# Optimization experiments

Measured on AMD Instinct MI355X. Metric: run time of the kernel, lower is better.

Reference implementation:

```python
import jax, jax.numpy as jnp
import numpy as np

N_NODE = 200000
HIDDEN = 128
BATCH = 1024
SEQ = 50
NNZ = 3200000
HG_STEPS = 3
LINE_STEPS = 3
BETA = 0.01
POS_MAX = 200


def setup_inputs() -> dict:
    key = jax.random.key(0)
    ks = jax.random.split(key, 20)
    stdv = 1.0 / np.sqrt(HIDDEN)
    u = lambda k, shp: jax.random.uniform(k, shp, jnp.float32, -stdv, stdv)
    inp = {
        "items_emb": u(ks[0], (N_NODE, HIDDEN)),
        "pos_table": u(ks[1], (POS_MAX, HIDDEN)),
        "w1_W": u(ks[2], (2 * HIDDEN, HIDDEN)), "w1_b": u(ks[3], (HIDDEN,)),
        "w2_W": u(ks[4], (HIDDEN, HIDDEN)), "w2_b": u(ks[5], (HIDDEN,)),
        "w3_W": u(ks[6], (HIDDEN, HIDDEN)), "w3_b": u(ks[7], (HIDDEN,)),
        "f_T": u(ks[8], (HIDDEN, 1)),
        "hg_vals": jax.random.uniform(ks[9], (NNZ,), jnp.float32),
        "line_adj_matrix": jax.random.uniform(ks[10], (BATCH, BATCH), jnp.float32),
        "degree": jax.random.uniform(ks[11], (BATCH, BATCH), jnp.float32),
        "hg_rows": jax.random.randint(ks[12], (NNZ,), 0, N_NODE, jnp.int32),
        "hg_cols": jax.random.randint(ks[13], (NNZ,), 0, N_NODE, jnp.int32),
        "session_info": jax.random.randint(ks[14], (BATCH, SEQ), 0, N_NODE, jnp.int64),
        "reversed_info": jax.random.randint(ks[15], (BATCH, SEQ), 0, N_NODE, jnp.int64),
        "sessions_len": jax.random.randint(ks[16], (BATCH,), 1, SEQ + 1, jnp.int32),
        "masks": jnp.ones((BATCH, SEQ), dtype=bool),
        "perm_row": jax.random.permutation(ks[17], BATCH).astype(jnp.int32),
        "perm_col": jax.random.permutation(ks[18], HIDDEN).astype(jnp.int32),
    }
    return inp


def _hypergraph_conv(rows, cols, vals, x):
    embs = x
    acc = x
    for _ in range(HG_STEPS):
        embs = jax.ops.segment_sum(vals[:, None] * embs[cols], rows, num_segments=N_NODE)
        acc = acc + embs
    return acc / (HG_STEPS + 1)


def _generate_hg_emb(item_emb, sessions_len, reversed_info, masks,
                     pos_table, w1_W, w1_b, w2_W, w2_b, w3_W, w3_b, f_T):
    padded = jnp.concatenate([jnp.zeros((1, HIDDEN), jnp.float32), item_emb], 0)
    seq_h = padded[reversed_info]                       # [B, L, H]
    L = seq_h.shape[1]
    slen = sessions_len.astype(jnp.float32)[:, None]
    sess_mean = jnp.sum(seq_h, 1) / slen                # [B, H]
    pos = pos_table[:L][None, :, :]                     # [1, L, H]
    new_seq = jnp.tanh(jnp.concatenate([jnp.broadcast_to(pos, seq_h.shape), seq_h], -1) @ w1_W + w1_b)
    gate = jax.nn.sigmoid((sess_mean @ w2_W + w2_b)[:, None, :] + new_seq @ w3_W + w3_b)
    alpha = (gate @ f_T) * masks.astype(jnp.float32)[:, :, None]   # [B, L, 1]
    theta = jnp.sum(alpha * new_seq, 1)                 # [B, H]
    return theta


def _line_graph_conv(D, A, items_emb, session_info, sessions_len):
    DA = D @ A
    padded = jnp.concatenate([jnp.zeros((1, HIDDEN), jnp.float32), items_emb], 0)
    sess = jnp.sum(padded[session_info], 1) / sessions_len.astype(jnp.float32)[:, None]
    acc = sess
    cur = sess
    for _ in range(LINE_STEPS):
        cur = DA @ cur
        acc = acc + cur
    return acc / (LINE_STEPS + 1)


def _ssl(hg_sess, line_sess, perm_row, perm_col):
    pos = jnp.sum(hg_sess * line_sess, 1)
    corrupted = hg_sess[perm_row][:, perm_col]
    neg = jnp.sum(corrupted * line_sess, 1)
    eps = 1e-08
    return jnp.sum(-jnp.log(eps + jax.nn.sigmoid(pos)) - jnp.log(eps + (1.0 - jax.nn.sigmoid(neg))))


def reference(items_emb, pos_table, w1_W, w1_b, w2_W, w2_b, w3_W, w3_b, f_T,
              hg_vals, line_adj_matrix, degree,
              hg_rows, hg_cols, session_info, reversed_info, sessions_len,
              masks, perm_row, perm_col):
    hg_item = _hypergraph_conv(hg_rows, hg_cols, hg_vals, items_emb)
    hg_sess = _generate_hg_emb(hg_item, sessions_len, reversed_info, masks,
                               pos_table, w1_W, w1_b, w2_W, w2_b, w3_W, w3_b, f_T)
    line_sess = _line_graph_conv(degree, line_adj_matrix, items_emb, session_info, sessions_len)
    cl_loss = BETA * _ssl(hg_sess, line_sess, perm_row, perm_col)
    return hg_sess, cl_loss, hg_item
```

## Files before the change

kernel.cpp:

```cpp
#include <hip/hip_runtime.h>
#include <hip/hip_fp16.h>
#include <cstdint>
#include <cstddef>

#define NN   200000
#define HH   128
#define BB   1024
#define LL   50
#define NNZK 3200000
#define RPBK 200
#define NBK  1000
#define MSB  256
#define CHUNK (NNZK/MSB)
#define SK   8

typedef unsigned int uint32;
typedef unsigned short ushort16;
typedef __attribute__((ext_vector_type(8))) short bf16x8;
typedef __attribute__((ext_vector_type(4))) float f32x4;
union U8 { uint32 u[4]; bf16x8 v; };

#if defined(__has_builtin)
#if __has_builtin(__builtin_amdgcn_cvt_pk_f32_fp8) && __has_builtin(__builtin_amdgcn_cvt_pk_fp8_f32)
#define HW_FP8 1
#endif
#endif
#ifndef HW_FP8
#define HW_FP8 0
#endif

__device__ __forceinline__ uint32 f2bf2(float a, float b){
  uint32 ua=__float_as_uint(a), ub=__float_as_uint(b);
  ua = (ua + 0x7FFFu + ((ua>>16)&1u)) >> 16;
  ub = (ub + 0x7FFFu + ((ub>>16)&1u)) >> 16;
  return ua | (ub<<16);
}
__device__ __forceinline__ float2 bf2x2f(uint32 u){
  return make_float2(__uint_as_float(u<<16), __uint_as_float(u & 0xFFFF0000u));
}

#if !HW_FP8
__device__ __forceinline__ uint32 enc8_sw(float f){
  ushort16 b = __half_as_ushort(__float2half_rn(f*0.00390625f));
  uint32 t = b & 0x7FFFu;
  uint32 r = (t + 0x3Fu + ((t>>7)&1u)) >> 7;
  if(r > 0x7Eu) r = 0x7Eu;
  return ((b>>8)&0x80u) | r;
}
#endif

__device__ __forceinline__ float2 fp8x2f(uint32 s){
#if HW_FP8
  auto r = __builtin_amdgcn_cvt_pk_f32_fp8((int)s, false);
  return make_float2(r[0], r[1]);
#else
  union{uint32 u; __half2 h;} cv;
  cv.u = ((s&0x80u)<<8)|((s&0x7Fu)<<7) | ((s&0x8000u)<<16)|((s&0x7F00u)<<15);
  float2 f = __half22float2(cv.h);
  return make_float2(f.x*256.f, f.y*256.f);
#endif
}

__device__ __forceinline__ ushort16 f2fp8x2(float a, float b){
#if HW_FP8
  return (ushort16)__builtin_amdgcn_cvt_pk_fp8_f32(a, b, 0, false);
#else
  return (ushort16)(enc8_sw(a) | (enc8_sw(b)<<8));
#endif
}

__device__ __forceinline__ uint32 f2fp8x4(float4 v){
#if HW_FP8
  int p = __builtin_amdgcn_cvt_pk_fp8_f32(v.x, v.y, 0, false);
  p = __builtin_amdgcn_cvt_pk_fp8_f32(v.z, v.w, p, true);
  return (uint32)p;
#else
  return enc8_sw(v.x) | (enc8_sw(v.y)<<8) | (enc8_sw(v.z)<<16) | (enc8_sw(v.w)<<24);
#endif
}

__global__ __launch_bounds__(256) void k_cvt_bhist(const float* __restrict__ x,
    uint32* __restrict__ obf, uint32* __restrict__ o8,
    const int* __restrict__ rows, int* __restrict__ bhist, int* __restrict__ bh2){
  if(blockIdx.x < MSB){
    __shared__ int h[NBK];
    for(int b=threadIdx.x;b<NBK;b+=256) h[b]=0;
    __syncthreads();
    const int i0=blockIdx.x*CHUNK;
    for(int i=i0+threadIdx.x;i<i0+CHUNK;i+=256) atomicAdd(&h[rows[i]/RPBK],1);
    __syncthreads();
    for(int b=threadIdx.x;b<NBK;b+=256){
      int c=h[b];
      bh2[blockIdx.x*NBK+b]=c;
      if(c) atomicAdd(&bhist[b],c);
    }
  } else {
    const int n = NN*32;
    const int nb = gridDim.x - MSB;
    for(int i=(blockIdx.x-MSB)*256+threadIdx.x; i<n; i+=nb*256){
      float4 v = ((const float4*)x)[i];
      obf[2*i]   = f2bf2(v.x, v.y);
      obf[2*i+1] = f2bf2(v.z, v.w);
      o8[i] = f2fp8x4(v);
    }
  }
}

__global__ __launch_bounds__(1024) void k_bscan(const int* __restrict__ bhist,
    int* __restrict__ bstart, int* __restrict__ bcur){
  __shared__ int s[1024];
  int t=threadIdx.x;
  int v=(t<NBK)?bhist[t]:0;
  s[t]=v;
  __syncthreads();
  for(int off=1;off<1024;off<<=1){
    int u=(t>=off)?s[t-off]:0; __syncthreads(); s[t]+=u; __syncthreads();
  }
  if(t<NBK){ int e=s[t]-v; bstart[t]=e; bcur[t]=e; }
}

__global__ __launch_bounds__(256) void k_msplit(const int* __restrict__ rows,
    const int* __restrict__ cols, const float* __restrict__ vals,
    const int* __restrict__ bh2, int* __restrict__ bcur, int2* __restrict__ bpk){
  __shared__ int hist[NBK];
  __shared__ int rbase[NBK];
  const int tid=threadIdx.x;
  const int i0=blockIdx.x*CHUNK, i1=i0+CHUNK;
  for(int b=tid;b<NBK;b+=256){
    int c=bh2[blockIdx.x*NBK+b];
    rbase[b] = c ? atomicAdd(&bcur[b],c) : 0;
    hist[b]=0;
  }
  __syncthreads();
  for(int i=i0+tid;i<i1;i+=256){
    int r=rows[i];
    int b=r/RPBK, ro=r-b*RPBK;
    int p = rbase[b] + atomicAdd(&hist[b],1);
    bpk[p]=make_int2(cols[i] | (ro<<18), __float_as_int(vals[i]));
  }
}

__global__ __launch_bounds__(256) void k_bucket_sort(const int2* __restrict__ bpk,
    const int* __restrict__ bstart, const int* __restrict__ bhist,
    int2* __restrict__ pk, int* __restrict__ rp){
  __shared__ int cnt[RPBK];
  __shared__ int sc[256];
  int b=blockIdx.x, t=threadIdx.x;
  int base=bstart[b], total=bhist[b];
  if(t<RPBK) cnt[t]=0;
  __syncthreads();
  for(int j=t;j<total;j+=256) atomicAdd(&cnt[((uint32)bpk[base+j].x)>>18],1);
  __syncthreads();
  int myc=(t<RPBK)?cnt[t]:0;
  sc[t]=myc;
  __syncthreads();
  for(int off=1;off<256;off<<=1){
    int u=(t>=off)?sc[t-off]:0; __syncthreads(); sc[t]+=u; __syncthreads();
  }
  int excl = sc[t]-myc;
  __syncthreads();
  if(t<RPBK){ cnt[t]=base+excl; rp[b*RPBK+t]=base+excl; }
  if(b==0 && t==0) rp[NN]=NNZK;
  __syncthreads();
  for(int j=t;j<total;j+=256){
    int2 e=bpk[base+j];
    int ro=((uint32)e.x)>>18;
    int p=atomicAdd(&cnt[ro],1);
    pk[p]=make_int2((e.x&0x3FFFF)<<7, e.y);
  }
}

__device__ __forceinline__ void spmm_body(const int2* __restrict__ pk, int j0, int j1,
    const char* __restrict__ src, int lane2, float& ax, float& ay){
  int j  = __builtin_amdgcn_readfirstlane(j0);
  int jE = __builtin_amdgcn_readfirstlane(j1);
  for(; j+16<=jE; j+=16){
    int2 p[16]; ushort16 e[16];
    #pragma unroll
    for(int u=0;u<16;++u) p[u]=pk[j+u];
    #pragma unroll
    for(int u=0;u<16;++u) e[u]=*(const ushort16*)(src + (uint32)__builtin_amdgcn_readfirstlane(p[u].x) + lane2);
    #pragma unroll
    for(int u=0;u<16;++u){
      float2 f=fp8x2f(e[u]);
      float v=__int_as_float(p[u].y);
      ax=fmaf(v,f.x,ax); ay=fmaf(v,f.y,ay);
    }
  }
  for(; j+8<=jE; j+=8){
    int2 p[8]; ushort16 e[8];
    #pragma unroll
    for(int u=0;u<8;++u) p[u]=pk[j+u];
    #pragma unroll
    for(int u=0;u<8;++u) e[u]=*(const ushort16*)(src + (uint32)__builtin_amdgcn_readfirstlane(p[u].x) + lane2);
    #pragma unroll
    for(int u=0;u<8;++u){
      float2 f=fp8x2f(e[u]);
      float v=__int_as_float(p[u].y);
      ax=fmaf(v,f.x,ax); ay=fmaf(v,f.y,ay);
    }
  }
  for(; j+4<=jE; j+=4){
    int2 p[4]; ushort16 e[4];
    #pragma unroll
    for(int u=0;u<4;++u) p[u]=pk[j+u];
    #pragma unroll
    for(int u=0;u<4;++u) e[u]=*(const ushort16*)(src + (uint32)__builtin_amdgcn_readfirstlane(p[u].x) + lane2);
    #pragma unroll
    for(int u=0;u<4;++u){
      float2 f=fp8x2f(e[u]);
      float v=__int_as_float(p[u].y);
      ax=fmaf(v,f.x,ax); ay=fmaf(v,f.y,ay);
    }
  }
  for(; j<jE; ++j){
    int2 p=pk[j];
    float2 f=fp8x2f(*(const ushort16*)(src + (uint32)__builtin_amdgcn_readfirstlane(p.x) + lane2));
    float v=__int_as_float(p.y);
    ax=fmaf(v,f.x,ax); ay=fmaf(v,f.y,ay);
  }
}

__global__ __launch_bounds__(256) void k_spmm_b(
    const int2* __restrict__ pk, const int* __restrict__ rp,
    const ushort16* __restrict__ src, ushort16* __restrict__ dst)
{
  int wid = blockIdx.x*4 + (threadIdx.x>>6);
  int lane = threadIdx.x & 63;
  if(wid>=NN) return;
  float ax=0.f, ay=0.f;
  spmm_body(pk, rp[wid], rp[wid+1], (const char*)src, lane*2, ax, ay);
  dst[(size_t)wid*64+lane]=f2fp8x2(ax,ay);
}

__global__ __launch_bounds__(256) void k_spmm_final(
    const int2* __restrict__ pk, const int* __restrict__ rp,
    const ushort16* __restrict__ A8, const ushort16* __restrict__ B8,
    const uint32* xbf, float* __restrict__ acc, uint32* obf)
{
  int wid = blockIdx.x*4 + (threadIdx.x>>6);
  int lane = threadIdx.x & 63;
  if(wid>=NN) return;
  float ax=0.f, ay=0.f;
  spmm_body(pk, rp[wid], rp[wid+1], (const char*)B8, lane*2, ax, ay);
  float2 xv  = bf2x2f(xbf[(size_t)wid*64+lane]);
  float2 e1v = fp8x2f(A8[(size_t)wid*64+lane]);
  float2 e2v = fp8x2f(B8[(size_t)wid*64+lane]);
  size_t ao=(size_t)wid*128 + lane*2;
  float rx = (xv.x + e1v.x + e2v.x + ax)*0.25f;
  float ry = (xv.y + e1v.y + e2v.y + ay)*0.25f;
  acc[ao]=rx; acc[ao+1]=ry;
  obf[(size_t)wid*64+lane]=f2bf2(rx,ry);
}

__global__ __launch_bounds__(128) void k_sessmean2(const uint32* __restrict__ hgbf,
    const int* __restrict__ rev, const int* __restrict__ slen,
    const float* __restrict__ w2, const float* __restrict__ b2, float* __restrict__ sm2,
    const float* __restrict__ pos_table, const float* __restrict__ w1W,
    const float* __restrict__ w1b0, float* __restrict__ posW1,
    const float* __restrict__ items, const int* __restrict__ sinfo,
    float* __restrict__ cur, float* __restrict__ accL){
  __shared__ float sm[HH];
  int b=blockIdx.x, h=threadIdx.x;
  int hw=h>>1, hi=h&1;
  float sl=1.f/(float)slen[b];
  {
    float s=0.f;
    for(int l=0;l<LL;++l){
      int idx=sinfo[b*LL+l];
      if(idx>0 && idx<=NN) s += items[(size_t)(idx-1)*HH+h];
    }
    s *= sl;
    cur[(size_t)b*HH+h]=s; accL[(size_t)b*HH+h]=s;
  }
  float s=0.f;
  for(int l=0;l<LL;++l){
    int idx=rev[b*LL+l];
    if(idx>0 && idx<=NN){
      float2 f=bf2x2f(hgbf[(size_t)(idx-1)*64+hw]);
      s += hi ? f.y : f.x;
    }
  }
  sm[h]=s*sl;
  __syncthreads();
  float a=b2[h];
  for(int k=0;k<HH;++k) a=fmaf(sm[k], w2[k*HH+h], a);
  sm2[b*HH+h]=a;
  if(b<LL){
    float pa=w1b0[h];
    for(int k=0;k<HH;++k) pa=fmaf(pos_table[b*HH+k], w1W[k*HH+h], pa);
    posW1[b*HH+h]=pa;
  }
}

#define AS 69
#define BS 67
__global__ __launch_bounds__(256) void k_nsgemm(
    const uint32* __restrict__ hgbf, const int* __restrict__ rev,
    const float* __restrict__ w1b, const float* __restrict__ posW1,
    float* __restrict__ ns)
{
  __shared__ uint32 sA[64*AS];
  __shared__ uint32 sB[128*BS];
  const int tid=threadIdx.x;
  {
    int r=tid>>2, p=tid&3;
    int idx = rev[blockIdx.x*64 + r];
    if(idx>0 && idx<=NN){
      const uint32* s = hgbf + (size_t)(idx-1)*64 + p*16;
      #pragma unroll
      for(int j=0;j<16;++j) sA[r*AS+p*16+j]=s[j];
    } else {
      #pragma unroll
      for(int j=0;j<16;++j) sA[r*AS+p*16+j]=0u;
    }
  }
  for(int i=tid;i<128*64;i+=256){
    int n=i&127, kp=i>>7;
    sB[n*BS+kp]=f2bf2(w1b[(2*kp)*HH+n], w1b[(2*kp+1)*HH+n]);
  }
  __syncthreads();
  const int w=tid>>6, lane=tid&63, g=lane>>4, m15=lane&15;
  f32x4 acc[8];
  #pragma unroll
  for(int nt=0;nt<8;++nt) acc[nt]=(f32x4){0.f,0.f,0.f,0.f};
  #pragma unroll
  for(int kt=0;kt<4;++kt){
    U8 a;
    int ab=(w*16+m15)*AS + kt*16 + g*4;
    a.u[0]=sA[ab]; a.u[1]=sA[ab+1]; a.u[2]=sA[ab+2]; a.u[3]=sA[ab+3];
    #pragma unroll
    for(int nt=0;nt<8;++nt){
      U8 b;
      int bb=(nt*16+m15)*BS + kt*16 + g*4;
      b.u[0]=sB[bb]; b.u[1]=sB[bb+1]; b.u[2]=sB[bb+2]; b.u[3]=sB[bb+3];
      acc[nt]=__builtin_amdgcn_mfma_f32_16x16x32_bf16(a.v,b.v,acc[nt],0,0,0);
    }
  }
  int rowbase = blockIdx.x*64 + w*16 + g*4;
  #pragma unroll
  for(int r=0;r<4;++r){
    int gr=rowbase+r;
    int l=gr%LL;
    #pragma unroll
    for(int nt=0;nt<8;++nt){
      int col=nt*16+m15;
      ns[(size_t)gr*HH+col] = tanhf(acc[nt][r] + posW1[l*HH+col]);
    }
  }
}

__global__ __launch_bounds__(256) void k_agemm(
    const float* __restrict__ ns, const float* __restrict__ w3,
    const float* __restrict__ sm2, const float* __restrict__ b3,
    const float* __restrict__ fT, float* __restrict__ alpha)
{
  __shared__ uint32 sA[64*AS];
  __shared__ uint32 sB[128*BS];
  const int tid=threadIdx.x;
  {
    int r=tid>>2, p=tid&3;
    const float2* s = (const float2*)(ns + (size_t)(blockIdx.x*64+r)*HH + p*32);
    #pragma unroll
    for(int j=0;j<16;++j){ float2 f=s[j]; sA[r*AS+p*16+j]=f2bf2(f.x,f.y); }
  }
  for(int i=tid;i<128*64;i+=256){
    int n=i&127, kp=i>>7;
    sB[n*BS+kp]=f2bf2(w3[(2*kp)*HH+n], w3[(2*kp+1)*HH+n]);
  }
  __syncthreads();
  const int w=tid>>6, lane=tid&63, g=lane>>4, m15=lane&15;
  f32x4 acc[8];
  #pragma unroll
  for(int nt=0;nt<8;++nt) acc[nt]=(f32x4){0.f,0.f,0.f,0.f};
  #pragma unroll
  for(int kt=0;kt<4;++kt){
    U8 a;
    int ab=(w*16+m15)*AS + kt*16 + g*4;
    a.u[0]=sA[ab]; a.u[1]=sA[ab+1]; a.u[2]=sA[ab+2]; a.u[3]=sA[ab+3];
    #pragma unroll
    for(int nt=0;nt<8;++nt){
      U8 b;
      int bb=(nt*16+m15)*BS + kt*16 + g*4;
      b.u[0]=sB[bb]; b.u[1]=sB[bb+1]; b.u[2]=sB[bb+2]; b.u[3]=sB[bb+3];
      acc[nt]=__builtin_amdgcn_mfma_f32_16x16x32_bf16(a.v,b.v,acc[nt],0,0,0);
    }
  }
  int rowbase = blockIdx.x*64 + w*16 + g*4;
  #pragma unroll
  for(int r=0;r<4;++r){
    int gr=rowbase+r;
    int b_=gr/LL;
    float rsum=0.f;
    #pragma unroll
    for(int nt=0;nt<8;++nt){
      int col=nt*16+m15;
      float gv = acc[nt][r] + sm2[b_*HH+col] + b3[col];
      rsum += fT[col] / (1.f + expf(-gv));
    }
    rsum += __shfl_xor(rsum,1);
    rsum += __shfl_xor(rsum,2);
    rsum += __shfl_xor(rsum,4);
    rsum += __shfl_xor(rsum,8);
    if(m15==0) alpha[gr]=rsum;
  }
}

__global__ __launch_bounds__(128) void k_theta(const float* __restrict__ ns,
    const float* __restrict__ alpha, float* __restrict__ hg_sess){
  __shared__ float sal[64];
  int b=blockIdx.x, h=threadIdx.x;
  if(h<LL) sal[h]=alpha[b*LL+h];
  __syncthreads();
  float t=0.f;
  for(int l=0;l<LL;++l) t=fmaf(sal[l], ns[((size_t)b*LL+l)*HH+h], t);
  hg_sess[(size_t)b*HH+h]=t;
}

__global__ __launch_bounds__(128) void k_matpart(const float* __restrict__ M,
    const float* __restrict__ src, float* __restrict__ part){
  int rq = blockIdx.x >> 3;
  int kc = blockIdx.x & 7;
  int h = threadIdx.x;
  int r0 = rq*4;
  const int KC = BB/SK;
  const float* m0 = M + (size_t)r0*BB + kc*KC;
  const float* m1 = m0 + BB;
  const float* m2 = m1 + BB;
  const float* m3 = m2 + BB;
  const float* s0 = src + (size_t)kc*KC*HH + h;
  float a0=0,a1=0,a2=0,a3=0;
  for(int k=0;k<KC;++k){
    float s=s0[(size_t)k*HH];
    a0=fmaf(m0[k],s,a0); a1=fmaf(m1[k],s,a1);
    a2=fmaf(m2[k],s,a2); a3=fmaf(m3[k],s,a3);
  }
  size_t o=(size_t)kc*BB*HH + (size_t)r0*HH + h;
  part[o]=a0; part[o+HH]=a1; part[o+2*HH]=a2; part[o+3*HH]=a3;
}

__global__ __launch_bounds__(256) void k_matcomb(const float* __restrict__ part,
    float* __restrict__ dst, float* __restrict__ acc, int mode){
  int i = blockIdx.x*256+threadIdx.x;
  const int S = BB*HH;
  float v = 0.f;
  #pragma unroll
  for(int kc=0;kc<SK;++kc) v += part[i+(size_t)kc*S];
  dst[i]=v;
  if(mode==1) acc[i]+=v;
  else if(mode==2) acc[i]=(acc[i]+v)*0.25f;
}

__global__ __launch_bounds__(128) void k_ssl(const float* __restrict__ hg,
    const float* __restrict__ line, const int* __restrict__ pr,
    const int* __restrict__ pc, float* __restrict__ part){
  int b=blockIdx.x, h=threadIdx.x;
  __shared__ float sp[2][2];
  float lv = line[(size_t)b*HH+h];
  float v1 = hg[(size_t)b*HH+h]*lv;
  float v2 = hg[(size_t)pr[b]*HH + pc[h]]*lv;
  for(int o=32;o>0;o>>=1){ v1+=__shfl_xor(v1,o); v2+=__shfl_xor(v2,o); }
  int wv=h>>6, ln=h&63;
  if(ln==0){ sp[0][wv]=v1; sp[1][wv]=v2; }
  __syncthreads();
  if(h==0){
    float pos=sp[0][0]+sp[0][1];
    float neg=sp[1][0]+sp[1][1];
    float sigp=1.f/(1.f+expf(-pos));
    float sign_=1.f/(1.f+expf(-neg));
    part[b] = -logf(1e-8f+sigp) - logf(1e-8f+(1.f-sign_));
  }
}

__global__ __launch_bounds__(256) void k_red(const float* __restrict__ part, float* __restrict__ loss){
  __shared__ float s[256];
  int t=threadIdx.x;
  s[t]=part[t]+part[t+256]+part[t+512]+part[t+768];
  __syncthreads();
  for(int o=128;o>0;o>>=1){ if(t<o) s[t]+=s[t+o]; __syncthreads(); }
  if(t==0) *loss = 0.01f*s[0];
}

extern "C" void kernel_launch(void* const* d_in, const int* in_sizes, int n_in,
                              void* d_out, int out_size, void* d_ws, size_t ws_size,
                              hipStream_t stream){
  const float* items    =(const float*)d_in[0];
  const float* pos_table=(const float*)d_in[1];
  const float* w1W      =(const float*)d_in[2];
  const float* w1b_     =(const float*)d_in[3];
  const float* w2W      =(const float*)d_in[4];
  const float* w2b      =(const float*)d_in[5];
  const float* w3W      =(const float*)d_in[6];
  const float* w3b      =(const float*)d_in[7];
  const float* fT       =(const float*)d_in[8];
  const float* hvals    =(const float*)d_in[9];
  const float* lineA    =(const float*)d_in[10];
  const float* degD     =(const float*)d_in[11];
  const int*   hrows    =(const int*)d_in[12];
  const int*   hcols    =(const int*)d_in[13];
  const int*   sinfo    =(const int*)d_in[14];
  const int*   rinfo    =(const int*)d_in[15];
  const int*   slen     =(const int*)d_in[16];
  const int*   prow     =(const int*)d_in[18];
  const int*   pcol     =(const int*)d_in[19];

  float* outf   = (float*)d_out;
  float* hg_sess= outf;
  float* loss   = outf + (size_t)BB*HH;
  float* hgout  = outf + (size_t)BB*HH + 1;

  char* base=(char*)d_ws; size_t off=0;
  auto carve=[&](size_t bytes)->char*{ char* p=base+off; off=(off+bytes+255)&~(size_t)255; return p; };

  float*    posW1 =(float*)   carve((size_t)LL*HH*4);
  float*    curA  =(float*)   carve((size_t)BB*HH*4);
  float*    curB  =(float*)   carve((size_t)BB*HH*4);
  float*    tmpv  =(float*)   carve((size_t)BB*HH*4);
  float*    accL  =(float*)   carve((size_t)BB*HH*4);
  float*    lpart =(float*)   carve((size_t)BB*4);
  float*    mpart =(float*)   carve((size_t)SK*BB*HH*4);
  int2*     pk    =(int2*)    carve((size_t)NNZK*8);
  int*      rp    =(int*)     carve((size_t)(NN+1)*4);
  int*      bhist =(int*)     carve((size_t)NBK*4);
  int*      bstart=(int*)     carve((size_t)NBK*4);
  int*      bcur  =(int*)     carve((size_t)NBK*4);
  int*      bh2   =(int*)     carve((size_t)MSB*NBK*4);
  uint32*   itbf  =(uint32*)  carve((size_t)NN*64*4);
  uint32*   it8   =(uint32*)  carve((size_t)NN*32*4);
  ushort16* A8    =(ushort16*)carve((size_t)NN*64*2);
  ushort16* B8    =(ushort16*)carve((size_t)NN*64*2);
  if(off > ws_size) return;

  int2*   bpk   = (int2*)A8;
  uint32* hgbf  = itbf;
  float*  ns    = (float*)A8;
  float*  alpha = ns + (size_t)BB*LL*HH;
  float*  sm2   = alpha + (size_t)BB*LL;

  hipMemsetAsync(bhist,0,(size_t)NBK*4,stream);
  k_cvt_bhist<<<MSB+2048,256,0,stream>>>(items,itbf,it8,hrows,bhist,bh2);
  k_bscan<<<1,1024,0,stream>>>(bhist,bstart,bcur);
  k_msplit<<<MSB,256,0,stream>>>(hrows,hcols,hvals,bh2,bcur,bpk);
  k_bucket_sort<<<NBK,256,0,stream>>>(bpk,bstart,bhist,pk,rp);

  k_spmm_b    <<<NN/4,256,0,stream>>>(pk,rp, (const ushort16*)it8, A8);
  k_spmm_b    <<<NN/4,256,0,stream>>>(pk,rp, A8, B8);
  k_spmm_final<<<NN/4,256,0,stream>>>(pk,rp, A8, B8, itbf, hgout, hgbf);

  k_sessmean2<<<BB,HH,0,stream>>>(hgbf,rinfo,slen,w2W,w2b,sm2,
                                  pos_table,w1W,w1b_,posW1,
                                  items,sinfo,curA,accL);
  k_nsgemm   <<<(BB*LL)/64,256,0,stream>>>(hgbf,rinfo,w1W+HH*HH,posW1,ns);
  k_agemm    <<<(BB*LL)/64,256,0,stream>>>(ns,w3W,sm2,w3b,fT,alpha);
  k_theta    <<<BB,HH,0,stream>>>(ns,alpha,hg_sess);

  for(int s=0;s<3;++s){
    float* srcv=(s&1)?curB:curA;
    float* dstv=(s&1)?curA:curB;
    k_matpart<<<(BB/4)*SK,128,0,stream>>>(lineA,srcv,mpart);
    k_matcomb<<<BB*HH/256,256,0,stream>>>(mpart,tmpv,nullptr,0);
    k_matpart<<<(BB/4)*SK,128,0,stream>>>(degD,tmpv,mpart);
    k_matcomb<<<BB*HH/256,256,0,stream>>>(mpart,dstv,accL,(s==2)?2:1);
  }

  k_ssl<<<BB,HH,0,stream>>>(hg_sess,accL,prow,pcol,lpart);
  k_red<<<1,256,0,stream>>>(lpart,loss);
}
```

Before: 602.1 us.

## Split SpMM wavefront into four nonzero groups with 8-byte fp8 loads

The SpMM kernels now split each row's wavefront into four 16-lane groups. Each group handles a different nonzero, loads 8 fp8 values (8 bytes) per lane, and accumulates 8 partial sums. The groups are then combined with cross-lane shuffles and only group 0 writes the output. The aim is to keep four independent gathers in flight per wavefront instead of one serialized wide gather per nonzero, improving memory-level parallelism on the random gathers. The cost is extra shuffle reductions, more registers, and three-quarters of the lanes idle during the epilogue.

```diff
diff --git a/kernel.cpp b/kernel.cpp
--- a/kernel.cpp
+++ b/kernel.cpp
@@ -170,87 +170,100 @@
   }
 }
 
-__device__ __forceinline__ void spmm_body(const int2* __restrict__ pk, int j0, int j1,
-    const char* __restrict__ src, int lane2, float& ax, float& ay){
+__device__ __forceinline__ void q_acc(float* ax, uint2 e, float v){
+  float2 f0=fp8x2f(e.x), f1=fp8x2f(e.x>>16);
+  float2 f2=fp8x2f(e.y), f3=fp8x2f(e.y>>16);
+  ax[0]=fmaf(v,f0.x,ax[0]); ax[1]=fmaf(v,f0.y,ax[1]);
+  ax[2]=fmaf(v,f1.x,ax[2]); ax[3]=fmaf(v,f1.y,ax[3]);
+  ax[4]=fmaf(v,f2.x,ax[4]); ax[5]=fmaf(v,f2.y,ax[5]);
+  ax[6]=fmaf(v,f3.x,ax[6]); ax[7]=fmaf(v,f3.y,ax[7]);
+}
+
+__device__ __forceinline__ void spmm_body_q(const int2* __restrict__ pk, int j0, int j1,
+    const char* __restrict__ src, int goff, int grp, float* ax){
   int j  = __builtin_amdgcn_readfirstlane(j0);
   int jE = __builtin_amdgcn_readfirstlane(j1);
   for(; j+16<=jE; j+=16){
-    int2 p[16]; ushort16 e[16];
-    #pragma unroll
-    for(int u=0;u<16;++u) p[u]=pk[j+u];
-    #pragma unroll
-    for(int u=0;u<16;++u) e[u]=*(const ushort16*)(src + (uint32)__builtin_amdgcn_readfirstlane(p[u].x) + lane2);
-    #pragma unroll
-    for(int u=0;u<16;++u){
-      float2 f=fp8x2f(e[u]);
-      float v=__int_as_float(p[u].y);
-      ax=fmaf(v,f.x,ax); ay=fmaf(v,f.y,ay);
-    }
-  }
-  for(; j+8<=jE; j+=8){
-    int2 p[8]; ushort16 e[8];
-    #pragma unroll
-    for(int u=0;u<8;++u) p[u]=pk[j+u];
-    #pragma unroll
-    for(int u=0;u<8;++u) e[u]=*(const ushort16*)(src + (uint32)__builtin_amdgcn_readfirstlane(p[u].x) + lane2);
-    #pragma unroll
-    for(int u=0;u<8;++u){
-      float2 f=fp8x2f(e[u]);
-      float v=__int_as_float(p[u].y);
-      ax=fmaf(v,f.x,ax); ay=fmaf(v,f.y,ay);
-    }
+    int2 p[4]; uint2 e[4];
+    #pragma unroll
+    for(int u=0;u<4;++u) p[u]=pk[j+4*u+grp];
+    #pragma unroll
+    for(int u=0;u<4;++u) e[u]=*(const uint2*)(src + (uint32)p[u].x + goff);
+    #pragma unroll
+    for(int u=0;u<4;++u) q_acc(ax, e[u], __int_as_float(p[u].y));
   }
   for(; j+4<=jE; j+=4){
-    int2 p[4]; ushort16 e[4];
-    #pragma unroll
-    for(int u=0;u<4;++u) p[u]=pk[j+u];
-    #pragma unroll
-    for(int u=0;u<4;++u) e[u]=*(const ushort16*)(src + (uint32)__builtin_amdgcn_readfirstlane(p[u].x) + lane2);
-    #pragma unroll
-    for(int u=0;u<4;++u){
-      float2 f=fp8x2f(e[u]);
-      float v=__int_as_float(p[u].y);
-      ax=fmaf(v,f.x,ax); ay=fmaf(v,f.y,ay);
-    }
-  }
-  for(; j<jE; ++j){
-    int2 p=pk[j];
-    float2 f=fp8x2f(*(const ushort16*)(src + (uint32)__builtin_amdgcn_readfirstlane(p.x) + lane2));
-    float v=__int_as_float(p.y);
-    ax=fmaf(v,f.x,ax); ay=fmaf(v,f.y,ay);
+    int2 p=pk[j+grp];
+    uint2 e=*(const uint2*)(src + (uint32)p.x + goff);
+    q_acc(ax, e, __int_as_float(p.y));
+  }
+  int rem = jE - j;
+  if(rem>0){
+    int jj = j + (grp<rem ? grp : 0);
+    int2 p=pk[jj];
+    float v = (grp<rem) ? __int_as_float(p.y) : 0.f;
+    uint2 e=*(const uint2*)(src + (uint32)p.x + goff);
+    q_acc(ax, e, v);
+  }
+}
+
+__device__ __forceinline__ void q_reduce(float* ax){
+  #pragma unroll
+  for(int k=0;k<8;++k){
+    ax[k] += __shfl_xor(ax[k],16);
+    ax[k] += __shfl_xor(ax[k],32);
   }
 }
 
 __global__ __launch_bounds__(256) void k_spmm_b(
     const int2* __restrict__ pk, const int* __restrict__ rp,
-    const ushort16* __restrict__ src, ushort16* __restrict__ dst)
+    const char* __restrict__ src, uint32* __restrict__ dst)
 {
   int wid = blockIdx.x*4 + (threadIdx.x>>6);
   int lane = threadIdx.x & 63;
   if(wid>=NN) return;
-  float ax=0.f, ay=0.f;
-  spmm_body(pk, rp[wid], rp[wid+1], (const char*)src, lane*2, ax, ay);
-  dst[(size_t)wid*64+lane]=f2fp8x2(ax,ay);
+  int grp=lane>>4, goff=(lane&15)*8;
+  float ax[8]={0,0,0,0,0,0,0,0};
+  spmm_body_q(pk, rp[wid], rp[wid+1], src, goff, grp, ax);
+  q_reduce(ax);
+  if(grp==0){
+    uint2 o;
+    o.x=f2fp8x4(make_float4(ax[0],ax[1],ax[2],ax[3]));
+    o.y=f2fp8x4(make_float4(ax[4],ax[5],ax[6],ax[7]));
+    *(uint2*)((char*)dst + (size_t)wid*128 + goff) = o;
+  }
 }
 
 __global__ __launch_bounds__(256) void k_spmm_final(
     const int2* __restrict__ pk, const int* __restrict__ rp,
-    const ushort16* __restrict__ A8, const ushort16* __restrict__ B8,
+    const char* __restrict__ A8, const char* __restrict__ B8,
     const uint32* xbf, float* __restrict__ acc, uint32* obf)
 {
   int wid = blockIdx.x*4 + (threadIdx.x>>6);
   int lane = threadIdx.x & 63;
   if(wid>=NN) return;
-  float ax=0.f, ay=0.f;
-  spmm_body(pk, rp[wid], rp[wid+1], (const char*)B8, lane*2, ax, ay);
-  float2 xv  = bf2x2f(xbf[(size_t)wid*64+lane]);
-  float2 e1v = fp8x2f(A8[(size_t)wid*64+lane]);
-  float2 e2v = fp8x2f(B8[(size_t)wid*64+lane]);
-  size_t ao=(size_t)wid*128 + lane*2;
-  float rx = (xv.x + e1v.x + e2v.x + ax)*0.25f;
-  float ry = (xv.y + e1v.y + e2v.y + ay)*0.25f;
-  acc[ao]=rx; acc[ao+1]=ry;
-  obf[(size_t)wid*64+lane]=f2bf2(rx,ry);
+  int grp=lane>>4, goff=(lane&15)*8;
+  float ax[8]={0,0,0,0,0,0,0,0};
+  spmm_body_q(pk, rp[wid], rp[wid+1], B8, goff, grp, ax);
+  q_reduce(ax);
+  if(grp==0){
+    uint2 e1=*(const uint2*)(A8 + (size_t)wid*128 + goff);
+    uint2 e2=*(const uint2*)(B8 + (size_t)wid*128 + goff);
+    float2 a0=fp8x2f(e1.x), a1=fp8x2f(e1.x>>16), a2=fp8x2f(e1.y), a3=fp8x2f(e1.y>>16);
+    float2 b0=fp8x2f(e2.x), b1=fp8x2f(e2.x>>16), b2=fp8x2f(e2.y), b3=fp8x2f(e2.y>>16);
+    int xi = wid*64 + (lane&15)*4;
+    uint32 x0=xbf[xi], x1=xbf[xi+1], x2=xbf[xi+2], x3=xbf[xi+3];
+    float2 xv0=bf2x2f(x0), xv1=bf2x2f(x1), xv2=bf2x2f(x2), xv3=bf2x2f(x3);
+    float r0=(xv0.x+a0.x+b0.x+ax[0])*0.25f, r1=(xv0.y+a0.y+b0.y+ax[1])*0.25f;
+    float r2=(xv1.x+a1.x+b1.x+ax[2])*0.25f, r3=(xv1.y+a1.y+b1.y+ax[3])*0.25f;
+    float r4=(xv2.x+a2.x+b2.x+ax[4])*0.25f, r5=(xv2.y+a2.y+b2.y+ax[5])*0.25f;
+    float r6=(xv3.x+a3.x+b3.x+ax[6])*0.25f, r7=(xv3.y+a3.y+b3.y+ax[7])*0.25f;
+    size_t ao=(size_t)wid*128 + (lane&15)*8;
+    acc[ao]=r0; acc[ao+1]=r1; acc[ao+2]=r2; acc[ao+3]=r3;
+    acc[ao+4]=r4; acc[ao+5]=r5; acc[ao+6]=r6; acc[ao+7]=r7;
+    obf[xi]  =f2bf2(r0,r1); obf[xi+1]=f2bf2(r2,r3);
+    obf[xi+2]=f2bf2(r4,r5); obf[xi+3]=f2bf2(r6,r7);
+  }
 }
 
 __global__ __launch_bounds__(128) void k_sessmean2(const uint32* __restrict__ hgbf,
@@ -527,8 +540,8 @@
   int*      bh2   =(int*)     carve((size_t)MSB*NBK*4);
   uint32*   itbf  =(uint32*)  carve((size_t)NN*64*4);
   uint32*   it8   =(uint32*)  carve((size_t)NN*32*4);
-  ushort16* A8    =(ushort16*)carve((size_t)NN*64*2);
-  ushort16* B8    =(ushort16*)carve((size_t)NN*64*2);
+  char*     A8    =(char*)    carve((size_t)NN*128);
+  char*     B8    =(char*)    carve((size_t)NN*128);
   if(off > ws_size) return;
 
   int2*   bpk   = (int2*)A8;
@@ -543,8 +556,8 @@
   k_msplit<<<MSB,256,0,stream>>>(hrows,hcols,hvals,bh2,bcur,bpk);
   k_bucket_sort<<<NBK,256,0,stream>>>(bpk,bstart,bhist,pk,rp);
 
-  k_spmm_b    <<<NN/4,256,0,stream>>>(pk,rp, (const ushort16*)it8, A8);
-  k_spmm_b    <<<NN/4,256,0,stream>>>(pk,rp, A8, B8);
+  k_spmm_b    <<<NN/4,256,0,stream>>>(pk,rp, (const char*)it8, (uint32*)A8);
+  k_spmm_b    <<<NN/4,256,0,stream>>>(pk,rp, A8, (uint32*)B8);
   k_spmm_final<<<NN/4,256,0,stream>>>(pk,rp, A8, B8, itbf, hgout, hgbf);
 
   k_sessmean2<<<BB,HH,0,stream>>>(hgbf,rinfo,slen,w2W,w2b,sm2,
```

Result: slower. 657.9 us (+9.3%).
